# Optimization experiments

Hardware: AMD Instinct MI355X
Metric: run time of the kernel (lower is better)

The kernel has to match this reference:

```python
import jax, jax.numpy as jnp
import numpy as np

ALPHA = 0.2  # LeakyReLU negative slope
N_NODES = 50000
N_EDGES = 800000
D_IN = 128
D_OUT = 128


def setup_inputs() -> dict:
    key = jax.random.key(0)
    k1, k2, k3, k4 = jax.random.split(key, 4)
    features = jax.random.normal(k1, (N_NODES, D_IN), dtype=jnp.float32)
    # xavier_normal gain=0.02 as in reset_parameters_xavier
    weight = jax.random.normal(k2, (D_IN, D_OUT), dtype=jnp.float32) * (0.02 * np.sqrt(2.0 / (D_IN + D_OUT)))
    a = jax.random.normal(k3, (2 * D_OUT, 1), dtype=jnp.float32) * np.sqrt(2.0 * 2.0 / (2 * D_OUT + 1))
    bias = jnp.zeros((D_OUT,), dtype=jnp.float32)
    adj_idx = jax.random.randint(k4, (2, N_EDGES), 0, N_NODES, dtype=jnp.int32)
    return {"features": features, "weight": weight, "a": a, "bias": bias, "adj_idx": adj_idx}


def reference(features, weight, a, bias, adj_idx):
    # h = X W + b   [N, D_OUT]
    h = jnp.dot(features, weight) + bias
    d = h.shape[1]
    # concat([h[src], h[dst]]) @ a  ==  (h @ a_src)[src] + (h @ a_dst)[dst]
    a_src = a[:d, 0]   # [D_OUT]
    a_dst = a[d:, 0]   # [D_OUT]
    s_node_src = jnp.dot(h, a_src)  # [N]
    s_node_dst = jnp.dot(h, a_dst)  # [N]
    src = adj_idx[0]
    dst = adj_idx[1]
    e = jax.nn.leaky_relu(s_node_src[src] + s_node_dst[dst], negative_slope=ALPHA)  # [E]
    # NOTE: original forward does NOT apply softmax to edge scores; spmm with raw scores.
    # out[i] = sum_{(i,j) in E} e_ij * h[j]
    out = jax.ops.segment_sum(e[:, None] * h[dst], src, num_segments=h.shape[0])
    return out
```

## Files before the change

### kernel.cpp

```cpp
#include <hip/hip_runtime.h>

constexpr int N_NODES = 50000;
constexpr int N_EDGES = 800000;
constexpr int D = 128;
constexpr float ALPHA = 0.2f;
constexpr int SCAN_NBLK = (N_NODES + 255) / 256;
constexpr int GEMM_NBLK = (N_NODES + 31) / 32;
constexpr int NXCD = 8;
constexpr int NODES_PER_G = N_NODES / NXCD;
constexpr int EDGE_NBLK = (N_EDGES + 255) / 256;

__device__ __forceinline__ void fma4(float4& acc, float s, const float4& w) {
    acc.x += s * w.x; acc.y += s * w.y; acc.z += s * w.z; acc.w += s * w.w;
}
__device__ __forceinline__ float dot4(const float4& x, const float4& y) {
    return x.x * y.x + x.y * y.y + x.z * y.z + x.w * y.w;
}
__device__ __forceinline__ unsigned bf16pack2(float a, float b) {
    unsigned ua = __float_as_uint(a); ua += 0x7FFFu + ((ua >> 16) & 1u);
    unsigned ub = __float_as_uint(b); ub += 0x7FFFu + ((ub >> 16) & 1u);
    return (ua >> 16) | (ub & 0xFFFF0000u);
}
__device__ __forceinline__ float bf16lo(unsigned p) { return __uint_as_float(p << 16); }
__device__ __forceinline__ float bf16hi(unsigned p) { return __uint_as_float(p & 0xFFFF0000u); }

__global__ __launch_bounds__(256)
void k_gemm_scores(const float* __restrict__ feat,
                   const float* __restrict__ W,
                   const float* __restrict__ a,
                   const float* __restrict__ bias,
                   uint2* __restrict__ hb,
                   float* __restrict__ s_src,
                   float* __restrict__ s_dst)
{
    __shared__ float4 w_lds[D * 32];
    const int tid = threadIdx.x;
    const float4* W4 = reinterpret_cast<const float4*>(W);
    #pragma unroll
    for (int i = 0; i < 16; ++i)
        w_lds[tid + i * 256] = W4[tid + i * 256];
    __syncthreads();

    const int cg = tid & 31;
    const int ng = tid >> 5;
    const int n0 = blockIdx.x * 32 + ng * 4;

    const float4 a_s = reinterpret_cast<const float4*>(a)[cg];
    const float4 a_d = reinterpret_cast<const float4*>(a)[32 + cg];
    const float4 b4  = reinterpret_cast<const float4*>(bias)[cg];

    const float4* fA = reinterpret_cast<const float4*>(feat) + (long long)min(n0 + 0, N_NODES - 1) * 32;
    const float4* fB = reinterpret_cast<const float4*>(feat) + (long long)min(n0 + 1, N_NODES - 1) * 32;
    const float4* fC = reinterpret_cast<const float4*>(feat) + (long long)min(n0 + 2, N_NODES - 1) * 32;
    const float4* fD = reinterpret_cast<const float4*>(feat) + (long long)min(n0 + 3, N_NODES - 1) * 32;

    float4 acc0 = {0.f, 0.f, 0.f, 0.f};
    float4 acc1 = {0.f, 0.f, 0.f, 0.f};
    float4 acc2 = {0.f, 0.f, 0.f, 0.f};
    float4 acc3 = {0.f, 0.f, 0.f, 0.f};

    #pragma unroll 4
    for (int kc = 0; kc < 32; ++kc) {
        const float4 fa = fA[kc];
        const float4 fb = fB[kc];
        const float4 fc = fC[kc];
        const float4 fd = fD[kc];
        const float4 w0 = w_lds[(kc * 4 + 0) * 32 + cg];
        const float4 w1 = w_lds[(kc * 4 + 1) * 32 + cg];
        const float4 w2 = w_lds[(kc * 4 + 2) * 32 + cg];
        const float4 w3 = w_lds[(kc * 4 + 3) * 32 + cg];
        fma4(acc0, fa.x, w0); fma4(acc0, fa.y, w1); fma4(acc0, fa.z, w2); fma4(acc0, fa.w, w3);
        fma4(acc1, fb.x, w0); fma4(acc1, fb.y, w1); fma4(acc1, fb.z, w2); fma4(acc1, fb.w, w3);
        fma4(acc2, fc.x, w0); fma4(acc2, fc.y, w1); fma4(acc2, fc.z, w2); fma4(acc2, fc.w, w3);
        fma4(acc3, fd.x, w0); fma4(acc3, fd.y, w1); fma4(acc3, fd.z, w2); fma4(acc3, fd.w, w3);
    }

    acc0.x += b4.x; acc0.y += b4.y; acc0.z += b4.z; acc0.w += b4.w;
    acc1.x += b4.x; acc1.y += b4.y; acc1.z += b4.z; acc1.w += b4.w;
    acc2.x += b4.x; acc2.y += b4.y; acc2.z += b4.z; acc2.w += b4.w;
    acc3.x += b4.x; acc3.y += b4.y; acc3.z += b4.z; acc3.w += b4.w;

    if (n0 + 0 < N_NODES) hb[(long long)(n0 + 0) * 32 + cg] = make_uint2(bf16pack2(acc0.x, acc0.y), bf16pack2(acc0.z, acc0.w));
    if (n0 + 1 < N_NODES) hb[(long long)(n0 + 1) * 32 + cg] = make_uint2(bf16pack2(acc1.x, acc1.y), bf16pack2(acc1.z, acc1.w));
    if (n0 + 2 < N_NODES) hb[(long long)(n0 + 2) * 32 + cg] = make_uint2(bf16pack2(acc2.x, acc2.y), bf16pack2(acc2.z, acc2.w));
    if (n0 + 3 < N_NODES) hb[(long long)(n0 + 3) * 32 + cg] = make_uint2(bf16pack2(acc3.x, acc3.y), bf16pack2(acc3.z, acc3.w));

    float ps0 = dot4(acc0, a_s), pd0 = dot4(acc0, a_d);
    float ps1 = dot4(acc1, a_s), pd1 = dot4(acc1, a_d);
    float ps2 = dot4(acc2, a_s), pd2 = dot4(acc2, a_d);
    float ps3 = dot4(acc3, a_s), pd3 = dot4(acc3, a_d);
    #pragma unroll
    for (int m = 1; m < 32; m <<= 1) {
        ps0 += __shfl_xor(ps0, m); pd0 += __shfl_xor(pd0, m);
        ps1 += __shfl_xor(ps1, m); pd1 += __shfl_xor(pd1, m);
        ps2 += __shfl_xor(ps2, m); pd2 += __shfl_xor(pd2, m);
        ps3 += __shfl_xor(ps3, m); pd3 += __shfl_xor(pd3, m);
    }
    if (cg == 0) {
        if (n0 + 0 < N_NODES) { s_src[n0 + 0] = ps0; s_dst[n0 + 0] = pd0; }
        if (n0 + 1 < N_NODES) { s_src[n0 + 1] = ps1; s_dst[n0 + 1] = pd1; }
        if (n0 + 2 < N_NODES) { s_src[n0 + 2] = ps2; s_dst[n0 + 2] = pd2; }
        if (n0 + 3 < N_NODES) { s_src[n0 + 3] = ps3; s_dst[n0 + 3] = pd3; }
    }
}

__global__ __launch_bounds__(256)
void k_hist(const int* __restrict__ adj, int* __restrict__ counts)
{
    const int g  = blockIdx.x & (NXCD - 1);
    const int eb = blockIdx.x >> 3;
    const int i  = eb * 256 + threadIdx.x;
    if (i >= N_EDGES) return;
    const int s = adj[i];
    if ((unsigned)(s - g * NODES_PER_G) < (unsigned)NODES_PER_G)
        atomicAdd(&counts[s], 1);
}

__device__ __forceinline__ int block_incl_scan(int v, int tid)
{
    __shared__ int wsum[4];
    const int lane = tid & 63;
    int x = v;
    #pragma unroll
    for (int off = 1; off < 64; off <<= 1) {
        const int y = __shfl_up(x, off);
        if (lane >= off) x += y;
    }
    if (lane == 63) wsum[tid >> 6] = x;
    __syncthreads();
    const int w = tid >> 6;
    int base = 0;
    #pragma unroll
    for (int k = 0; k < 3; ++k)
        if (k < w) base += wsum[k];
    return x + base;
}

__global__ __launch_bounds__(256)
void k_scan1(const int* __restrict__ counts,
             int* __restrict__ incl,
             int* __restrict__ bsum)
{
    const int i = blockIdx.x * 256 + threadIdx.x;
    const int v = (i < N_NODES) ? counts[i] : 0;
    const int x = block_incl_scan(v, threadIdx.x);
    if (i < N_NODES) incl[i] = x;
    if (threadIdx.x == 255) bsum[blockIdx.x] = x;
}

__global__ __launch_bounds__(256)
void k_scan2(const int* __restrict__ bsum, int* __restrict__ bbase)
{
    const int t = threadIdx.x;
    const int v = (t < SCAN_NBLK) ? bsum[t] : 0;
    const int x = block_incl_scan(v, t);
    if (t < SCAN_NBLK) bbase[t] = x - v;
}

__global__ __launch_bounds__(256)
void k_scan3(const int* __restrict__ incl,
             const int* __restrict__ counts,
             const int* __restrict__ bbase,
             int* __restrict__ row_start,
             int* __restrict__ cursor)
{
    const int i = blockIdx.x * 256 + threadIdx.x;
    if (i < N_NODES) {
        const int e = incl[i] - counts[i] + bbase[blockIdx.x];
        row_start[i] = e;
        cursor[i]    = e;
    }
}

__global__ __launch_bounds__(256)
void k_fill(const int* __restrict__ adj,
            int* __restrict__ cursor,
            int* __restrict__ col)
{
    const int g  = blockIdx.x & (NXCD - 1);
    const int eb = blockIdx.x >> 3;
    const int i  = eb * 256 + threadIdx.x;
    if (i >= N_EDGES) return;
    const int s = adj[i];
    if ((unsigned)(s - g * NODES_PER_G) < (unsigned)NODES_PER_G) {
        const int d = adj[N_EDGES + i];
        const int pos = atomicAdd(&cursor[s], 1);
        col[pos] = d;
    }
}

__global__ __launch_bounds__(256)
void k_gather(const int* __restrict__ row_start,
              const int* __restrict__ cursor,
              const int* __restrict__ col,
              const float* __restrict__ s_src,
              const float* __restrict__ s_dst,
              const uint2* __restrict__ hb,
              float* __restrict__ out)
{
    const int tid  = threadIdx.x;
    const int cg   = tid & 31;
    const int node = blockIdx.x * 8 + (tid >> 5);
    const int beg  = row_start[node];
    const int end  = cursor[node];
    const float ss = s_src[node];

    float4 acc = {0.f, 0.f, 0.f, 0.f};
    int j = beg;
    for (; j + 1 < end; j += 2) {
        const int d0 = col[j];
        const int d1 = col[j + 1];
        const float x0 = ss + s_dst[d0];
        const float x1 = ss + s_dst[d1];
        const float e0 = x0 > 0.f ? x0 : ALPHA * x0;
        const float e1 = x1 > 0.f ? x1 : ALPHA * x1;
        const uint2 p0 = hb[(long long)d0 * 32 + cg];
        const uint2 p1 = hb[(long long)d1 * 32 + cg];
        acc.x += e0 * bf16lo(p0.x) + e1 * bf16lo(p1.x);
        acc.y += e0 * bf16hi(p0.x) + e1 * bf16hi(p1.x);
        acc.z += e0 * bf16lo(p0.y) + e1 * bf16lo(p1.y);
        acc.w += e0 * bf16hi(p0.y) + e1 * bf16hi(p1.y);
    }
    if (j < end) {
        const int d0 = col[j];
        const float x0 = ss + s_dst[d0];
        const float e0 = x0 > 0.f ? x0 : ALPHA * x0;
        const uint2 p0 = hb[(long long)d0 * 32 + cg];
        acc.x += e0 * bf16lo(p0.x);
        acc.y += e0 * bf16hi(p0.x);
        acc.z += e0 * bf16lo(p0.y);
        acc.w += e0 * bf16hi(p0.y);
    }
    reinterpret_cast<float4*>(out)[(long long)node * 32 + cg] = acc;
}

extern "C" void kernel_launch(void* const* d_in, const int* in_sizes, int n_in,
                              void* d_out, int out_size, void* d_ws, size_t ws_size,
                              hipStream_t stream) {
    const float* feat = (const float*)d_in[0];
    const float* W    = (const float*)d_in[1];
    const float* a    = (const float*)d_in[2];
    const float* bias = (const float*)d_in[3];
    const int*   adj  = (const int*)d_in[4];
    float* out = (float*)d_out;

    char* ws = (char*)d_ws;
    uint2* hb        = (uint2*)(ws);
    float* s_src     = (float*)(ws + 25600000);
    float* s_dst     = (float*)(ws + 25800000);
    int*   counts    = (int*)  (ws + 26000000);
    int*   row_start = (int*)  (ws + 26200000);
    int*   cursor    = (int*)  (ws + 26400000);
    int*   col       = (int*)  (ws + 26600000);
    int*   incl      = col;
    int*   bsum      = (int*)  (ws + 29800000);
    int*   bbase     = (int*)  (ws + 29804096);

    hipMemsetAsync(counts, 0, N_NODES * sizeof(int), stream);

    k_gemm_scores<<<GEMM_NBLK, 256, 0, stream>>>(feat, W, a, bias, hb, s_src, s_dst);
    k_hist<<<EDGE_NBLK * NXCD, 256, 0, stream>>>(adj, counts);
    k_scan1<<<SCAN_NBLK, 256, 0, stream>>>(counts, incl, bsum);
    k_scan2<<<1, 256, 0, stream>>>(bsum, bbase);
    k_scan3<<<SCAN_NBLK, 256, 0, stream>>>(incl, counts, bbase, row_start, cursor);
    k_fill<<<EDGE_NBLK * NXCD, 256, 0, stream>>>(adj, cursor, col);
    k_gather<<<N_NODES / 8, 256, 0, stream>>>(row_start, cursor, col,
                                              s_src, s_dst, hb, out);
}
```

Before: 240.9 us.

## Fuse GEMM with edge histogram, store weights as bf16 in LDS, merge scan kernels

Merges the score GEMM and the source-degree histogram into one kernel launched with 1568 blocks. Each block does its 32-node GEMM tile and then grid-strides over edge chunks for its XCD group. The weight tile is packed to bf16 in LDS, halving its size so more blocks can be resident, at the cost of unpacking on every load and reduced weight precision. scan2 is folded into scan3: each block redundantly scans the block sums to get its own base, which removes one launch. A separate hazard: N_NODES/32 needs 1563 GEMM blocks and the grid is 1568, so coverage holds, but node coverage now depends on the grid size rather than being derived from N_NODES.

```diff
diff --git a/kernel.cpp b/kernel.cpp
--- a/kernel.cpp
+++ b/kernel.cpp
@@ -5,10 +5,11 @@
 constexpr int D = 128;
 constexpr float ALPHA = 0.2f;
 constexpr int SCAN_NBLK = (N_NODES + 255) / 256;
-constexpr int GEMM_NBLK = (N_NODES + 31) / 32;
 constexpr int NXCD = 8;
 constexpr int NODES_PER_G = N_NODES / NXCD;
 constexpr int EDGE_NBLK = (N_EDGES + 255) / 256;
+constexpr int FUSE_NBLK = 196 * NXCD;
+constexpr int HIST_STRIDE = FUSE_NBLK / NXCD;
 
 __device__ __forceinline__ void fma4(float4& acc, float s, const float4& w) {
     acc.x += s * w.x; acc.y += s * w.y; acc.z += s * w.z; acc.w += s * w.w;
@@ -24,21 +25,25 @@
 __device__ __forceinline__ float bf16lo(unsigned p) { return __uint_as_float(p << 16); }
 __device__ __forceinline__ float bf16hi(unsigned p) { return __uint_as_float(p & 0xFFFF0000u); }
 
-__global__ __launch_bounds__(256)
-void k_gemm_scores(const float* __restrict__ feat,
-                   const float* __restrict__ W,
-                   const float* __restrict__ a,
-                   const float* __restrict__ bias,
-                   uint2* __restrict__ hb,
-                   float* __restrict__ s_src,
-                   float* __restrict__ s_dst)
-{
-    __shared__ float4 w_lds[D * 32];
+__global__ __launch_bounds__(256, 4)
+void k_gemm_hist(const float* __restrict__ feat,
+                 const float* __restrict__ W,
+                 const float* __restrict__ a,
+                 const float* __restrict__ bias,
+                 uint2* __restrict__ hb,
+                 float* __restrict__ s_src,
+                 float* __restrict__ s_dst,
+                 const int* __restrict__ adj,
+                 int* __restrict__ counts)
+{
+    __shared__ uint2 w_lds[D * 32];
     const int tid = threadIdx.x;
     const float4* W4 = reinterpret_cast<const float4*>(W);
     #pragma unroll
-    for (int i = 0; i < 16; ++i)
-        w_lds[tid + i * 256] = W4[tid + i * 256];
+    for (int i = 0; i < 16; ++i) {
+        const float4 w = W4[tid + i * 256];
+        w_lds[tid + i * 256] = make_uint2(bf16pack2(w.x, w.y), bf16pack2(w.z, w.w));
+    }
     __syncthreads();
 
     const int cg = tid & 31;
@@ -65,10 +70,14 @@
         const float4 fb = fB[kc];
         const float4 fc = fC[kc];
         const float4 fd = fD[kc];
-        const float4 w0 = w_lds[(kc * 4 + 0) * 32 + cg];
-        const float4 w1 = w_lds[(kc * 4 + 1) * 32 + cg];
-        const float4 w2 = w_lds[(kc * 4 + 2) * 32 + cg];
-        const float4 w3 = w_lds[(kc * 4 + 3) * 32 + cg];
+        const uint2 p0 = w_lds[(kc * 4 + 0) * 32 + cg];
+        const uint2 p1 = w_lds[(kc * 4 + 1) * 32 + cg];
+        const uint2 p2 = w_lds[(kc * 4 + 2) * 32 + cg];
+        const uint2 p3 = w_lds[(kc * 4 + 3) * 32 + cg];
+        const float4 w0 = {bf16lo(p0.x), bf16hi(p0.x), bf16lo(p0.y), bf16hi(p0.y)};
+        const float4 w1 = {bf16lo(p1.x), bf16hi(p1.x), bf16lo(p1.y), bf16hi(p1.y)};
+        const float4 w2 = {bf16lo(p2.x), bf16hi(p2.x), bf16lo(p2.y), bf16hi(p2.y)};
+        const float4 w3 = {bf16lo(p3.x), bf16hi(p3.x), bf16lo(p3.y), bf16hi(p3.y)};
         fma4(acc0, fa.x, w0); fma4(acc0, fa.y, w1); fma4(acc0, fa.z, w2); fma4(acc0, fa.w, w3);
         fma4(acc1, fb.x, w0); fma4(acc1, fb.y, w1); fma4(acc1, fb.z, w2); fma4(acc1, fb.w, w3);
         fma4(acc2, fc.x, w0); fma4(acc2, fc.y, w1); fma4(acc2, fc.z, w2); fma4(acc2, fc.w, w3);
@@ -102,18 +111,16 @@
         if (n0 + 2 < N_NODES) { s_src[n0 + 2] = ps2; s_dst[n0 + 2] = pd2; }
         if (n0 + 3 < N_NODES) { s_src[n0 + 3] = ps3; s_dst[n0 + 3] = pd3; }
     }
-}
-
-__global__ __launch_bounds__(256)
-void k_hist(const int* __restrict__ adj, int* __restrict__ counts)
-{
-    const int g  = blockIdx.x & (NXCD - 1);
-    const int eb = blockIdx.x >> 3;
-    const int i  = eb * 256 + threadIdx.x;
-    if (i >= N_EDGES) return;
-    const int s = adj[i];
-    if ((unsigned)(s - g * NODES_PER_G) < (unsigned)NODES_PER_G)
-        atomicAdd(&counts[s], 1);
+
+    const int g = blockIdx.x & (NXCD - 1);
+    for (int eb = blockIdx.x >> 3; eb < EDGE_NBLK; eb += HIST_STRIDE) {
+        const int i = eb * 256 + tid;
+        if (i < N_EDGES) {
+            const int s = adj[i];
+            if ((unsigned)(s - g * NODES_PER_G) < (unsigned)NODES_PER_G)
+                atomicAdd(&counts[s], 1);
+        }
+    }
 }
 
 __device__ __forceinline__ int block_incl_scan(int v, int tid)
@@ -149,24 +156,21 @@
 }
 
 __global__ __launch_bounds__(256)
-void k_scan2(const int* __restrict__ bsum, int* __restrict__ bbase)
-{
+void k_scan3(const int* __restrict__ incl,
+             const int* __restrict__ counts,
+             const int* __restrict__ bsum,
+             int* __restrict__ row_start,
+             int* __restrict__ cursor)
+{
+    __shared__ int sbase;
     const int t = threadIdx.x;
     const int v = (t < SCAN_NBLK) ? bsum[t] : 0;
     const int x = block_incl_scan(v, t);
-    if (t < SCAN_NBLK) bbase[t] = x - v;
-}
-
-__global__ __launch_bounds__(256)
-void k_scan3(const int* __restrict__ incl,
-             const int* __restrict__ counts,
-             const int* __restrict__ bbase,
-             int* __restrict__ row_start,
-             int* __restrict__ cursor)
-{
-    const int i = blockIdx.x * 256 + threadIdx.x;
+    if (t == blockIdx.x) sbase = x - v;
+    __syncthreads();
+    const int i = blockIdx.x * 256 + t;
     if (i < N_NODES) {
-        const int e = incl[i] - counts[i] + bbase[blockIdx.x];
+        const int e = incl[i] - counts[i] + sbase;
         row_start[i] = e;
         cursor[i]    = e;
     }
@@ -254,15 +258,13 @@
     int*   col       = (int*)  (ws + 26600000);
     int*   incl      = col;
     int*   bsum      = (int*)  (ws + 29800000);
-    int*   bbase     = (int*)  (ws + 29804096);
 
     hipMemsetAsync(counts, 0, N_NODES * sizeof(int), stream);
 
-    k_gemm_scores<<<GEMM_NBLK, 256, 0, stream>>>(feat, W, a, bias, hb, s_src, s_dst);
-    k_hist<<<EDGE_NBLK * NXCD, 256, 0, stream>>>(adj, counts);
+    k_gemm_hist<<<FUSE_NBLK, 256, 0, stream>>>(feat, W, a, bias, hb, s_src, s_dst,
+                                               adj, counts);
     k_scan1<<<SCAN_NBLK, 256, 0, stream>>>(counts, incl, bsum);
-    k_scan2<<<1, 256, 0, stream>>>(bsum, bbase);
-    k_scan3<<<SCAN_NBLK, 256, 0, stream>>>(incl, counts, bbase, row_start, cursor);
+    k_scan3<<<SCAN_NBLK, 256, 0, stream>>>(incl, counts, bsum, row_start, cursor);
     k_fill<<<EDGE_NBLK * NXCD, 256, 0, stream>>>(adj, cursor, col);
     k_gather<<<N_NODES / 8, 256, 0, stream>>>(row_start, cursor, col,
                                               s_src, s_dst, hb, out);
```

Measured after the change: 244.3 us. Within noise of the previous version (+1.4%).
